# Kernel tuning notes

Measured on AMD Instinct MI355X. Metric: run time of the kernel, lower is better.

Reference implementation:

```python
import jax, jax.numpy as jnp
import numpy as np

N_NODES = 100000
N_EDGES = 1200000
N_GRAPHS = 256
IN_C, HID_C, OUT_C = 5, 64, 2


def gcn_conv(x, src, dst, W, b, n_nodes):
    """PyG GCNConv: h = x@W; add self-loops; deg from target col (edge weight 1);
    norm = deg^{-1/2}[src]*deg^{-1/2}[dst]; scatter-add messages into dst; + bias."""
    loop = jnp.arange(n_nodes, dtype=src.dtype)
    s = jnp.concatenate([src, loop])
    d = jnp.concatenate([dst, loop])
    deg = jax.ops.segment_sum(jnp.ones_like(d, dtype=x.dtype), d, num_segments=n_nodes)
    dinv = jnp.where(deg > 0, jax.lax.rsqrt(deg), 0.0)
    norm = dinv[s] * dinv[d]                     # [E+N]
    h = x @ W                                    # [N, out]
    msg = h[s] * norm[:, None]                   # gather + scale  [E+N, out]
    out = jax.ops.segment_sum(msg, d, num_segments=n_nodes)  # scatter-add
    return out + b


def setup_inputs() -> dict:
    key = jax.random.key(0)
    ks = jax.random.split(key, 10)
    x = jax.random.normal(ks[0], (N_NODES, IN_C), dtype=jnp.float32)
    edge_index = jax.random.randint(ks[1], (2, N_EDGES), 0, N_NODES, dtype=jnp.int64)
    batch = jnp.sort(jax.random.randint(ks[2], (N_NODES,), 0, N_GRAPHS, dtype=jnp.int64))
    def glorot(k, fan_in, fan_out):
        lim = np.sqrt(6.0 / (fan_in + fan_out))
        return jax.random.uniform(k, (fan_in, fan_out), jnp.float32, -lim, lim)
    W1 = glorot(ks[3], IN_C, HID_C)
    b1 = jnp.zeros((HID_C,), jnp.float32)
    W2 = glorot(ks[4], HID_C, HID_C)
    b2 = jnp.zeros((HID_C,), jnp.float32)
    Wfc = glorot(ks[5], HID_C, OUT_C)
    bfc = jnp.zeros((OUT_C,), jnp.float32)
    return {"x": x, "edge_index": edge_index, "batch": batch,
            "W1": W1, "b1": b1, "W2": W2, "b2": b2, "Wfc": Wfc, "bfc": bfc}


def reference(x, edge_index, batch, W1, b1, W2, b2, Wfc, bfc):
    src, dst = edge_index[0], edge_index[1]
    h = jax.nn.relu(gcn_conv(x, src, dst, W1, b1, N_NODES))
    h = jax.nn.relu(gcn_conv(h, src, dst, W2, b2, N_NODES))
    # global_mean_pool over graph ids in `batch`
    sums = jax.ops.segment_sum(h, batch, num_segments=N_GRAPHS)          # [G, H]
    cnts = jax.ops.segment_sum(jnp.ones((h.shape[0],), h.dtype), batch,
                               num_segments=N_GRAPHS)                    # [G]
    pooled = sums / jnp.maximum(cnts, 1.0)[:, None]
    return pooled @ Wfc + bfc                                            # [G, 2]
```

## Files before the change

### kernel.cpp

```cpp
#include <hip/hip_runtime.h>

#define N_NODES 100000
#define N_EDGES 1200000
#define N_GRAPHS 256
#define IN_C 5
#define HID_C 64
#define OUT_C 2

#define BSH 7
#define BNODES 128
#define NB ((N_NODES + BNODES - 1) / BNODES)
#define CAPB 2048
#define EPB 2048
#define NBLK_E ((N_EDGES + EPB - 1) / EPB)
#define GNPW 8
#define L1NPW 8

typedef unsigned int uint32;

__device__ __forceinline__ uint32 f2bf(float f) {
    uint32 x = __float_as_uint(f);
    return (x + 0x7FFFu + ((x >> 16) & 1u)) >> 16;
}
__device__ __forceinline__ float bflo(uint32 r) { return __uint_as_float(r << 16); }
__device__ __forceinline__ float bfhi(uint32 r) { return __uint_as_float(r & 0xFFFF0000u); }

__global__ void k_bscatter(const int* __restrict__ src, const int* __restrict__ dst,
                           int* __restrict__ bcnt, int* __restrict__ pairs,
                           float* __restrict__ pooled) {
    __shared__ int h[NB];
    if (blockIdx.x < (N_GRAPHS * HID_C) / 256)
        pooled[blockIdx.x * 256 + threadIdx.x] = 0.f;
    for (int i = threadIdx.x; i < NB; i += blockDim.x) h[i] = 0;
    __syncthreads();
    int e0 = blockIdx.x * EPB;
    int e1 = e0 + EPB; if (e1 > N_EDGES) e1 = N_EDGES;
    for (int e = e0 + threadIdx.x; e < e1; e += blockDim.x)
        atomicAdd(&h[dst[e] >> BSH], 1);
    __syncthreads();
    for (int i = threadIdx.x; i < NB; i += blockDim.x)
        if (h[i]) h[i] = (i << 11) + atomicAdd(&bcnt[i], h[i]);
    __syncthreads();
    for (int e = e0 + threadIdx.x; e < e1; e += blockDim.x) {
        int d = dst[e];
        int pos = atomicAdd(&h[d >> BSH], 1);
        pairs[pos] = ((d & (BNODES - 1)) << 17) | src[e];
    }
}

__global__ void k_bsort_xs(const int* __restrict__ pairs, const int* __restrict__ bcnt,
                           const float* __restrict__ x,
                           int* __restrict__ csr, int* __restrict__ rs,
                           int* __restrict__ cnt, float* __restrict__ dinv,
                           float* __restrict__ xs) {
    __shared__ int hist[BNODES];
    __shared__ int tmp[BNODES];
    __shared__ int cur[BNODES];
    __shared__ float sdv[BNODES];
    int b = blockIdx.x;
    int t = threadIdx.x;
    int base = b << BSH;
    if (t < BNODES) hist[t] = 0;
    __syncthreads();
    int s = b << 11;
    int n = bcnt[b];
    for (int i = t; i < n; i += 256)
        atomicAdd(&hist[pairs[s + i] >> 17], 1);
    __syncthreads();
    int v = (t < BNODES) ? hist[t] : 0;
    if (t < BNODES) tmp[t] = v;
    __syncthreads();
    for (int off = 1; off < BNODES; off <<= 1) {
        int a = (t < BNODES && t >= off) ? tmp[t - off] : 0;
        __syncthreads();
        if (t < BNODES) tmp[t] += a;
        __syncthreads();
    }
    float dv_t = rsqrtf((float)v + 1.0f);
    if (t < BNODES) {
        cur[t] = tmp[t] - v;
        sdv[t] = dv_t;
        if (base + t < N_NODES) {
            rs[base + t] = s + tmp[t] - v;
            cnt[base + t] = v;
            dinv[base + t] = dv_t;
        }
    }
    __syncthreads();
    for (int i = t; i < n; i += 256) {
        int p = pairs[s + i];
        int pos = atomicAdd(&cur[p >> 17], 1);
        csr[s + pos] = p & 0x1FFFF;
    }
    for (int i = t; i < BNODES * 8; i += 256) {
        int nl = i >> 3, k = i & 7;
        int node = base + nl;
        if (node < N_NODES && k < IN_C)
            xs[(unsigned)node * 8 + k] = x[(unsigned)node * IN_C + k] * sdv[nl];
    }
}

__global__ void __launch_bounds__(256) k_l1(
        const float* __restrict__ xs, const int* __restrict__ csr,
        const int* __restrict__ rs, const int* __restrict__ cnt,
        const float* __restrict__ dinv, const float* __restrict__ b1,
        const float* __restrict__ W1, const float* __restrict__ W2,
        uint32* __restrict__ g2t) {
    __shared__ __align__(16) float sagg[4][L1NPW][8];
    __shared__ __align__(16) float srow[4][2][HID_C];
    int tid = threadIdx.x;
    int w = tid >> 6;
    int lane = tid & 63;
    int base = (blockIdx.x * 4 + w) * L1NPW;

    int g = lane >> 3, l = lane & 7;
    int v = base + g;
    float a0 = 0.f, a1 = 0.f, a2 = 0.f, a3 = 0.f, a4 = 0.f;
    if (v < N_NODES) {
        int k0 = rs[v];
        int n = cnt[v];
        if (l == 0) {
            float4 p = *(const float4*)&xs[(unsigned)v * 8];
            a0 = p.x; a1 = p.y; a2 = p.z; a3 = p.w;
            a4 = xs[(unsigned)v * 8 + 4];
        }
        int i = l;
        int un = (i < n) ? csr[k0 + i] : -1;
        while (un >= 0) {
            int u = un;
            i += 8;
            un = (i < n) ? csr[k0 + i] : -1;
            float4 p = *(const float4*)&xs[(unsigned)u * 8];
            float p4 = xs[(unsigned)u * 8 + 4];
            a0 += p.x; a1 += p.y; a2 += p.z; a3 += p.w; a4 += p4;
        }
    }
#pragma unroll
    for (int off = 4; off; off >>= 1) {
        a0 += __shfl_xor(a0, off);
        a1 += __shfl_xor(a1, off);
        a2 += __shfl_xor(a2, off);
        a3 += __shfl_xor(a3, off);
        a4 += __shfl_xor(a4, off);
    }
    if (l == 0 && v < N_NODES) {
        *(float4*)&sagg[w][g][0] = make_float4(a0, a1, a2, a3);
        sagg[w][g][4] = a4;
    }

    int half = lane >> 5, c2 = lane & 31;
    int kb = half << 5;
    float2 w1r[IN_C];
#pragma unroll
    for (int k = 0; k < IN_C; ++k)
        w1r[k] = *(const float2*)&W1[k * HID_C + 2 * c2];
    float2 w2r[32];
#pragma unroll
    for (int j = 0; j < 32; ++j)
        w2r[j] = *(const float2*)&W2[(kb + j) * HID_C + 2 * c2];
    float2 bias = *(const float2*)&b1[2 * c2];

    for (int gg = 0; gg < L1NPW; ++gg) {
        int node = base + gg;
        if (node >= N_NODES) break;
        float dv = dinv[node];
        float4 qa = *(const float4*)&sagg[w][gg][0];
        float q4 = sagg[w][gg][4];
        float s0 = qa.x * w1r[0].x + qa.y * w1r[1].x + qa.z * w1r[2].x
                 + qa.w * w1r[3].x + q4 * w1r[4].x;
        float s1 = qa.x * w1r[0].y + qa.y * w1r[1].y + qa.z * w1r[2].y
                 + qa.w * w1r[3].y + q4 * w1r[4].y;
        float h0 = fmaxf(s0 * dv + bias.x, 0.f);
        float h1 = fmaxf(s1 * dv + bias.y, 0.f);
        int buf = gg & 1;
        if (half == 0) *(float2*)&srow[w][buf][2 * c2] = make_float2(h0, h1);
        float t0 = 0.f, t1 = 0.f;
#pragma unroll
        for (int jj = 0; jj < 8; ++jj) {
            float4 hv = *(const float4*)&srow[w][buf][kb + 4 * jj];
            t0 += hv.x * w2r[4 * jj + 0].x + hv.y * w2r[4 * jj + 1].x
                + hv.z * w2r[4 * jj + 2].x + hv.w * w2r[4 * jj + 3].x;
            t1 += hv.x * w2r[4 * jj + 0].y + hv.y * w2r[4 * jj + 1].y
                + hv.z * w2r[4 * jj + 2].y + hv.w * w2r[4 * jj + 3].y;
        }
        t0 += __shfl_xor(t0, 32);
        t1 += __shfl_xor(t1, 32);
        if (half == 0)
            g2t[(unsigned)node * 32 + c2] = (f2bf(t1 * dv) << 16) | f2bf(t0 * dv);
    }
}

#define LDU2(d, u) uint2 d = *(const uint2*)&g[(unsigned)(u) * 32 + 2 * c4]
#define ACC4(s0, s1, s2, s3, r) { s0 += bflo(r.x); s1 += bfhi(r.x); \
                                  s2 += bflo(r.y); s3 += bfhi(r.y); }
__global__ void __launch_bounds__(256, 4) k_gather2p(
        const uint32* __restrict__ g, const int* __restrict__ csr,
        const int* __restrict__ rs, const int* __restrict__ cnt,
        const float* __restrict__ dinv, const float* __restrict__ b,
        const int* __restrict__ batch, float* __restrict__ pooled) {
    int wv = __builtin_amdgcn_readfirstlane(
        blockIdx.x * (blockDim.x >> 6) + (threadIdx.x >> 6));
    int n0 = wv * GNPW;
    if (n0 >= N_NODES) return;
    int lane = threadIdx.x & 63;
    int sub = lane >> 4;
    int c4 = lane & 15;
    int va = n0 + sub, vb = n0 + 4 + sub;
    int ka = rs[va], na = cnt[va];
    int kb = rs[vb], nb = cnt[vb];
    float dva = dinv[va], dvb = dinv[vb];
    int ga = batch[va], gb = batch[vb];
    float4 bias = *(const float4*)&b[4 * c4];
    LDU2(rsa, va); LDU2(rsb, vb);
    float a0 = bflo(rsa.x), a1 = bfhi(rsa.x), a2 = bflo(rsa.y), a3 = bfhi(rsa.y);
    float y0 = bflo(rsb.x), y1 = bfhi(rsb.x), y2 = bflo(rsb.y), y3 = bfhi(rsb.y);
    int ia = 0, ib = 0;
    while (ia + 7 < na && ib + 7 < nb) {
        int u0 = csr[ka+ia+0], u1 = csr[ka+ia+1], u2 = csr[ka+ia+2], u3 = csr[ka+ia+3];
        int u4 = csr[ka+ia+4], u5 = csr[ka+ia+5], u6 = csr[ka+ia+6], u7 = csr[ka+ia+7];
        int w0 = csr[kb+ib+0], w1 = csr[kb+ib+1], w2 = csr[kb+ib+2], w3 = csr[kb+ib+3];
        int w4 = csr[kb+ib+4], w5 = csr[kb+ib+5], w6 = csr[kb+ib+6], w7 = csr[kb+ib+7];
        LDU2(p0, u0); LDU2(p1, u1); LDU2(p2, u2); LDU2(p3, u3);
        LDU2(p4, u4); LDU2(p5, u5); LDU2(p6, u6); LDU2(p7, u7);
        LDU2(q0, w0); LDU2(q1, w1); LDU2(q2, w2); LDU2(q3, w3);
        LDU2(q4, w4); LDU2(q5, w5); LDU2(q6, w6); LDU2(q7, w7);
        ACC4(a0, a1, a2, a3, p0); ACC4(a0, a1, a2, a3, p1);
        ACC4(a0, a1, a2, a3, p2); ACC4(a0, a1, a2, a3, p3);
        ACC4(a0, a1, a2, a3, p4); ACC4(a0, a1, a2, a3, p5);
        ACC4(a0, a1, a2, a3, p6); ACC4(a0, a1, a2, a3, p7);
        ACC4(y0, y1, y2, y3, q0); ACC4(y0, y1, y2, y3, q1);
        ACC4(y0, y1, y2, y3, q2); ACC4(y0, y1, y2, y3, q3);
        ACC4(y0, y1, y2, y3, q4); ACC4(y0, y1, y2, y3, q5);
        ACC4(y0, y1, y2, y3, q6); ACC4(y0, y1, y2, y3, q7);
        ia += 8; ib += 8;
    }
    while (ia + 7 < na) {
        int u0 = csr[ka+ia+0], u1 = csr[ka+ia+1], u2 = csr[ka+ia+2], u3 = csr[ka+ia+3];
        int u4 = csr[ka+ia+4], u5 = csr[ka+ia+5], u6 = csr[ka+ia+6], u7 = csr[ka+ia+7];
        LDU2(p0, u0); LDU2(p1, u1); LDU2(p2, u2); LDU2(p3, u3);
        LDU2(p4, u4); LDU2(p5, u5); LDU2(p6, u6); LDU2(p7, u7);
        ACC4(a0, a1, a2, a3, p0); ACC4(a0, a1, a2, a3, p1);
        ACC4(a0, a1, a2, a3, p2); ACC4(a0, a1, a2, a3, p3);
        ACC4(a0, a1, a2, a3, p4); ACC4(a0, a1, a2, a3, p5);
        ACC4(a0, a1, a2, a3, p6); ACC4(a0, a1, a2, a3, p7);
        ia += 8;
    }
    while (ib + 7 < nb) {
        int w0 = csr[kb+ib+0], w1 = csr[kb+ib+1], w2 = csr[kb+ib+2], w3 = csr[kb+ib+3];
        int w4 = csr[kb+ib+4], w5 = csr[kb+ib+5], w6 = csr[kb+ib+6], w7 = csr[kb+ib+7];
        LDU2(q0, w0); LDU2(q1, w1); LDU2(q2, w2); LDU2(q3, w3);
        LDU2(q4, w4); LDU2(q5, w5); LDU2(q6, w6); LDU2(q7, w7);
        ACC4(y0, y1, y2, y3, q0); ACC4(y0, y1, y2, y3, q1);
        ACC4(y0, y1, y2, y3, q2); ACC4(y0, y1, y2, y3, q3);
        ACC4(y0, y1, y2, y3, q4); ACC4(y0, y1, y2, y3, q5);
        ACC4(y0, y1, y2, y3, q6); ACC4(y0, y1, y2, y3, q7);
        ib += 8;
    }
    while (ia + 3 < na && ib + 3 < nb) {
        int u0 = csr[ka+ia+0], u1 = csr[ka+ia+1], u2 = csr[ka+ia+2], u3 = csr[ka+ia+3];
        int w0 = csr[kb+ib+0], w1 = csr[kb+ib+1], w2 = csr[kb+ib+2], w3 = csr[kb+ib+3];
        LDU2(p0, u0); LDU2(p1, u1); LDU2(p2, u2); LDU2(p3, u3);
        LDU2(q0, w0); LDU2(q1, w1); LDU2(q2, w2); LDU2(q3, w3);
        ACC4(a0, a1, a2, a3, p0); ACC4(a0, a1, a2, a3, p1);
        ACC4(a0, a1, a2, a3, p2); ACC4(a0, a1, a2, a3, p3);
        ACC4(y0, y1, y2, y3, q0); ACC4(y0, y1, y2, y3, q1);
        ACC4(y0, y1, y2, y3, q2); ACC4(y0, y1, y2, y3, q3);
        ia += 4; ib += 4;
    }
    while (ia + 3 < na) {
        int u0 = csr[ka+ia+0], u1 = csr[ka+ia+1], u2 = csr[ka+ia+2], u3 = csr[ka+ia+3];
        LDU2(p0, u0); LDU2(p1, u1); LDU2(p2, u2); LDU2(p3, u3);
        ACC4(a0, a1, a2, a3, p0); ACC4(a0, a1, a2, a3, p1);
        ACC4(a0, a1, a2, a3, p2); ACC4(a0, a1, a2, a3, p3);
        ia += 4;
    }
    while (ib + 3 < nb) {
        int w0 = csr[kb+ib+0], w1 = csr[kb+ib+1], w2 = csr[kb+ib+2], w3 = csr[kb+ib+3];
        LDU2(q0, w0); LDU2(q1, w1); LDU2(q2, w2); LDU2(q3, w3);
        ACC4(y0, y1, y2, y3, q0); ACC4(y0, y1, y2, y3, q1);
        ACC4(y0, y1, y2, y3, q2); ACC4(y0, y1, y2, y3, q3);
        ib += 4;
    }
    while (ia < na && ib < nb) {
        int u0 = csr[ka + ia], w0 = csr[kb + ib];
        LDU2(p0, u0); LDU2(q0, w0);
        ACC4(a0, a1, a2, a3, p0); ACC4(y0, y1, y2, y3, q0);
        ++ia; ++ib;
    }
    while (ia < na) {
        LDU2(p0, csr[ka + ia]);
        ACC4(a0, a1, a2, a3, p0);
        ++ia;
    }
    while (ib < nb) {
        LDU2(q0, csr[kb + ib]);
        ACC4(y0, y1, y2, y3, q0);
        ++ib;
    }
    float oa0 = fmaxf(a0 * dva + bias.x, 0.f);
    float oa1 = fmaxf(a1 * dva + bias.y, 0.f);
    float oa2 = fmaxf(a2 * dva + bias.z, 0.f);
    float oa3 = fmaxf(a3 * dva + bias.w, 0.f);
    float ob0 = fmaxf(y0 * dvb + bias.x, 0.f);
    float ob1 = fmaxf(y1 * dvb + bias.y, 0.f);
    float ob2 = fmaxf(y2 * dvb + bias.z, 0.f);
    float ob3 = fmaxf(y3 * dvb + bias.w, 0.f);
    int g0 = __builtin_amdgcn_readfirstlane(ga);
    if (__all(ga == g0) && __all(gb == g0)) {
        float f0 = oa0 + ob0, f1 = oa1 + ob1, f2 = oa2 + ob2, f3 = oa3 + ob3;
        f0 += __shfl_xor(f0, 16); f0 += __shfl_xor(f0, 32);
        f1 += __shfl_xor(f1, 16); f1 += __shfl_xor(f1, 32);
        f2 += __shfl_xor(f2, 16); f2 += __shfl_xor(f2, 32);
        f3 += __shfl_xor(f3, 16); f3 += __shfl_xor(f3, 32);
        if (sub == 0) {
            atomicAdd(&pooled[g0 * HID_C + 4 * c4 + 0], f0);
            atomicAdd(&pooled[g0 * HID_C + 4 * c4 + 1], f1);
            atomicAdd(&pooled[g0 * HID_C + 4 * c4 + 2], f2);
            atomicAdd(&pooled[g0 * HID_C + 4 * c4 + 3], f3);
        }
    } else {
        atomicAdd(&pooled[ga * HID_C + 4 * c4 + 0], oa0);
        atomicAdd(&pooled[ga * HID_C + 4 * c4 + 1], oa1);
        atomicAdd(&pooled[ga * HID_C + 4 * c4 + 2], oa2);
        atomicAdd(&pooled[ga * HID_C + 4 * c4 + 3], oa3);
        atomicAdd(&pooled[gb * HID_C + 4 * c4 + 0], ob0);
        atomicAdd(&pooled[gb * HID_C + 4 * c4 + 1], ob1);
        atomicAdd(&pooled[gb * HID_C + 4 * c4 + 2], ob2);
        atomicAdd(&pooled[gb * HID_C + 4 * c4 + 3], ob3);
    }
}

__global__ void k_fc(const float* __restrict__ pooled, const int* __restrict__ batch,
                     const float* __restrict__ Wfc, const float* __restrict__ bfc,
                     float* __restrict__ out) {
    int g = blockIdx.x;
    int c = threadIdx.x;
    int lo = 0, hi = N_NODES;
    while (lo < hi) { int mid = (lo + hi) >> 1; if (batch[mid] < g) lo = mid + 1; else hi = mid; }
    int start = lo;
    hi = N_NODES;
    while (lo < hi) { int mid = (lo + hi) >> 1; if (batch[mid] < g + 1) lo = mid + 1; else hi = mid; }
    int n = lo - start;
    float pv = pooled[g * HID_C + c] / (float)(n > 0 ? n : 1);
    float o0 = pv * Wfc[c * OUT_C + 0];
    float o1 = pv * Wfc[c * OUT_C + 1];
#pragma unroll
    for (int off = 32; off > 0; off >>= 1) {
        o0 += __shfl_down(o0, off);
        o1 += __shfl_down(o1, off);
    }
    if (c == 0) {
        out[g * OUT_C + 0] = o0 + bfc[0];
        out[g * OUT_C + 1] = o1 + bfc[1];
    }
}

extern "C" void kernel_launch(void* const* d_in, const int* in_sizes, int n_in,
                              void* d_out, int out_size, void* d_ws, size_t ws_size,
                              hipStream_t stream) {
    const float* x    = (const float*)d_in[0];
    const int*   ei   = (const int*)d_in[1];
    const int*   src  = ei;
    const int*   dst  = ei + N_EDGES;
    const int*   batch= (const int*)d_in[2];
    const float* W1   = (const float*)d_in[3];
    const float* b1   = (const float*)d_in[4];
    const float* W2   = (const float*)d_in[5];
    const float* b2   = (const float*)d_in[6];
    const float* Wfc  = (const float*)d_in[7];
    const float* bfc  = (const float*)d_in[8];
    float* out = (float*)d_out;

    float*  ws     = (float*)d_ws;
    int*    bcnt   = (int*)ws;
    float*  pooled = ws + 1024;
    float*  dinv   = pooled + 16384;
    int*    cnt    = (int*)(dinv + 100352);
    int*    rs     = cnt + 100352;
    int*    pairs  = rs + 100352;
    int*    csr    = pairs + (NB * CAPB);
    float*  xs     = (float*)(csr + (NB * CAPB));
    uint32* g2tab  = (uint32*)(xs + N_NODES * 8);

    hipMemsetAsync(bcnt, 0, 1024 * sizeof(int), stream);

    k_bscatter<<<NBLK_E, 256, 0, stream>>>(src, dst, bcnt, pairs, pooled);
    k_bsort_xs<<<NB, 256, 0, stream>>>(pairs, bcnt, x, csr, rs, cnt, dinv, xs);

    {
        int blocks = (N_NODES + 4 * L1NPW - 1) / (4 * L1NPW);
        k_l1<<<blocks, 256, 0, stream>>>(xs, csr, rs, cnt, dinv, b1, W1, W2, g2tab);
    }

    {
        int waves = (N_NODES + GNPW - 1) / GNPW;
        int blocks = (waves + 3) / 4;
        k_gather2p<<<blocks, 256, 0, stream>>>(g2tab, csr, rs, cnt, dinv, b2, batch, pooled);
    }

    k_fc<<<N_GRAPHS, 64, 0, stream>>>(pooled, batch, Wfc, bfc, out);
}
```

Measured before the change: 205.0 us.

## Split layer-2 feature table into channel slices mapped to XCD pairs

The bf16 layer-2 feature table is stored as four 16-channel slices instead of one 64-channel row per node. The gather kernel maps blocks so that each pair of XCDs handles one slice, which shrinks the working set each XCD's L2 must cache during random neighbour gathers. Each wave now processes 32 nodes with 4 lanes per node rather than 8 nodes with 16 lanes. The cost is four times as many CSR index reads and edge loops, plus extra shuffle reductions before the pooled atomics.

```diff
diff --git a/kernel.cpp b/kernel.cpp
--- a/kernel.cpp
+++ b/kernel.cpp
@@ -13,8 +13,8 @@
 #define CAPB 2048
 #define EPB 2048
 #define NBLK_E ((N_EDGES + EPB - 1) / EPB)
-#define GNPW 8
 #define L1NPW 8
+#define SLICE_W (N_NODES * 8)
 
 typedef unsigned int uint32;
 
@@ -159,6 +159,8 @@
     for (int j = 0; j < 32; ++j)
         w2r[j] = *(const float2*)&W2[(kb + j) * HID_C + 2 * c2];
     float2 bias = *(const float2*)&b1[2 * c2];
+    unsigned sbase = (unsigned)(c2 >> 3) * SLICE_W;
+    int wir = c2 & 7;
 
     for (int gg = 0; gg < L1NPW; ++gg) {
         int node = base + gg;
@@ -186,34 +188,41 @@
         t0 += __shfl_xor(t0, 32);
         t1 += __shfl_xor(t1, 32);
         if (half == 0)
-            g2t[(unsigned)node * 32 + c2] = (f2bf(t1 * dv) << 16) | f2bf(t0 * dv);
-    }
-}
-
-#define LDU2(d, u) uint2 d = *(const uint2*)&g[(unsigned)(u) * 32 + 2 * c4]
+            g2t[sbase + (unsigned)node * 8 + wir] = (f2bf(t1 * dv) << 16) | f2bf(t0 * dv);
+    }
+}
+
+#define LDU2(d, u) uint2 d = *(const uint2*)&gs[(unsigned)(u) * 8 + 2 * cq]
 #define ACC4(s0, s1, s2, s3, r) { s0 += bflo(r.x); s1 += bfhi(r.x); \
                                   s2 += bflo(r.y); s3 += bfhi(r.y); }
 __global__ void __launch_bounds__(256, 4) k_gather2p(
-        const uint32* __restrict__ g, const int* __restrict__ csr,
+        const uint32* __restrict__ g2s, const int* __restrict__ csr,
         const int* __restrict__ rs, const int* __restrict__ cnt,
         const float* __restrict__ dinv, const float* __restrict__ b,
         const int* __restrict__ batch, float* __restrict__ pooled) {
-    int wv = __builtin_amdgcn_readfirstlane(
-        blockIdx.x * (blockDim.x >> 6) + (threadIdx.x >> 6));
-    int n0 = wv * GNPW;
-    if (n0 >= N_NODES) return;
+    int blk = blockIdx.x;
+    int xcd = blk & 7;
+    int slice = xcd >> 1;
+    int sblk = ((blk >> 3) << 1) | (xcd & 1);
+    int w = threadIdx.x >> 6;
     int lane = threadIdx.x & 63;
-    int sub = lane >> 4;
-    int c4 = lane & 15;
-    int va = n0 + sub, vb = n0 + 4 + sub;
-    int ka = rs[va], na = cnt[va];
-    int kb = rs[vb], nb = cnt[vb];
-    float dva = dinv[va], dvb = dinv[vb];
-    int ga = batch[va], gb = batch[vb];
-    float4 bias = *(const float4*)&b[4 * c4];
-    LDU2(rsa, va); LDU2(rsb, vb);
-    float a0 = bflo(rsa.x), a1 = bfhi(rsa.x), a2 = bflo(rsa.y), a3 = bfhi(rsa.y);
-    float y0 = bflo(rsb.x), y1 = bfhi(rsb.x), y2 = bflo(rsb.y), y3 = bfhi(rsb.y);
+    int sub = lane >> 2;
+    int cq = lane & 3;
+    int n0 = sblk * BNODES + w * 32;
+    int va = n0 + sub, vb = n0 + 16 + sub;
+    int vva = va < N_NODES, vvb = vb < N_NODES;
+    int vca = vva ? va : N_NODES - 1;
+    int vcb = vvb ? vb : N_NODES - 1;
+    const uint32* gs = g2s + (unsigned)slice * SLICE_W;
+    int ka = rs[vca], na = vva ? cnt[vca] : 0;
+    int kb = rs[vcb], nb = vvb ? cnt[vcb] : 0;
+    float dva = dinv[vca], dvb = dinv[vcb];
+    int ga = batch[vca], gb = batch[vcb];
+    float4 bias = *(const float4*)&b[slice * 16 + 4 * cq];
+    float a0 = 0.f, a1 = 0.f, a2 = 0.f, a3 = 0.f;
+    float y0 = 0.f, y1 = 0.f, y2 = 0.f, y3 = 0.f;
+    if (vva) { LDU2(rsa, va); ACC4(a0, a1, a2, a3, rsa); }
+    if (vvb) { LDU2(rsb, vb); ACC4(y0, y1, y2, y3, rsb); }
     int ia = 0, ib = 0;
     while (ia + 7 < na && ib + 7 < nb) {
         int u0 = csr[ka+ia+0], u1 = csr[ka+ia+1], u2 = csr[ka+ia+2], u3 = csr[ka+ia+3];
@@ -297,36 +306,41 @@
         ACC4(y0, y1, y2, y3, q0);
         ++ib;
     }
-    float oa0 = fmaxf(a0 * dva + bias.x, 0.f);
-    float oa1 = fmaxf(a1 * dva + bias.y, 0.f);
-    float oa2 = fmaxf(a2 * dva + bias.z, 0.f);
-    float oa3 = fmaxf(a3 * dva + bias.w, 0.f);
-    float ob0 = fmaxf(y0 * dvb + bias.x, 0.f);
-    float ob1 = fmaxf(y1 * dvb + bias.y, 0.f);
-    float ob2 = fmaxf(y2 * dvb + bias.z, 0.f);
-    float ob3 = fmaxf(y3 * dvb + bias.w, 0.f);
+    float oa0 = vva ? fmaxf(a0 * dva + bias.x, 0.f) : 0.f;
+    float oa1 = vva ? fmaxf(a1 * dva + bias.y, 0.f) : 0.f;
+    float oa2 = vva ? fmaxf(a2 * dva + bias.z, 0.f) : 0.f;
+    float oa3 = vva ? fmaxf(a3 * dva + bias.w, 0.f) : 0.f;
+    float ob0 = vvb ? fmaxf(y0 * dvb + bias.x, 0.f) : 0.f;
+    float ob1 = vvb ? fmaxf(y1 * dvb + bias.y, 0.f) : 0.f;
+    float ob2 = vvb ? fmaxf(y2 * dvb + bias.z, 0.f) : 0.f;
+    float ob3 = vvb ? fmaxf(y3 * dvb + bias.w, 0.f) : 0.f;
     int g0 = __builtin_amdgcn_readfirstlane(ga);
+    int cb = slice * 16 + 4 * cq;
     if (__all(ga == g0) && __all(gb == g0)) {
         float f0 = oa0 + ob0, f1 = oa1 + ob1, f2 = oa2 + ob2, f3 = oa3 + ob3;
+        f0 += __shfl_xor(f0, 4); f0 += __shfl_xor(f0, 8);
         f0 += __shfl_xor(f0, 16); f0 += __shfl_xor(f0, 32);
+        f1 += __shfl_xor(f1, 4); f1 += __shfl_xor(f1, 8);
         f1 += __shfl_xor(f1, 16); f1 += __shfl_xor(f1, 32);
+        f2 += __shfl_xor(f2, 4); f2 += __shfl_xor(f2, 8);
         f2 += __shfl_xor(f2, 16); f2 += __shfl_xor(f2, 32);
+        f3 += __shfl_xor(f3, 4); f3 += __shfl_xor(f3, 8);
         f3 += __shfl_xor(f3, 16); f3 += __shfl_xor(f3, 32);
         if (sub == 0) {
-            atomicAdd(&pooled[g0 * HID_C + 4 * c4 + 0], f0);
-            atomicAdd(&pooled[g0 * HID_C + 4 * c4 + 1], f1);
-            atomicAdd(&pooled[g0 * HID_C + 4 * c4 + 2], f2);
-            atomicAdd(&pooled[g0 * HID_C + 4 * c4 + 3], f3);
+            atomicAdd(&pooled[g0 * HID_C + cb + 0], f0);
+            atomicAdd(&pooled[g0 * HID_C + cb + 1], f1);
+            atomicAdd(&pooled[g0 * HID_C + cb + 2], f2);
+            atomicAdd(&pooled[g0 * HID_C + cb + 3], f3);
         }
     } else {
-        atomicAdd(&pooled[ga * HID_C + 4 * c4 + 0], oa0);
-        atomicAdd(&pooled[ga * HID_C + 4 * c4 + 1], oa1);
-        atomicAdd(&pooled[ga * HID_C + 4 * c4 + 2], oa2);
-        atomicAdd(&pooled[ga * HID_C + 4 * c4 + 3], oa3);
-        atomicAdd(&pooled[gb * HID_C + 4 * c4 + 0], ob0);
-        atomicAdd(&pooled[gb * HID_C + 4 * c4 + 1], ob1);
-        atomicAdd(&pooled[gb * HID_C + 4 * c4 + 2], ob2);
-        atomicAdd(&pooled[gb * HID_C + 4 * c4 + 3], ob3);
+        atomicAdd(&pooled[ga * HID_C + cb + 0], oa0);
+        atomicAdd(&pooled[ga * HID_C + cb + 1], oa1);
+        atomicAdd(&pooled[ga * HID_C + cb + 2], oa2);
+        atomicAdd(&pooled[ga * HID_C + cb + 3], oa3);
+        atomicAdd(&pooled[gb * HID_C + cb + 0], ob0);
+        atomicAdd(&pooled[gb * HID_C + cb + 1], ob1);
+        atomicAdd(&pooled[gb * HID_C + cb + 2], ob2);
+        atomicAdd(&pooled[gb * HID_C + cb + 3], ob3);
     }
 }
 
@@ -392,11 +406,7 @@
         k_l1<<<blocks, 256, 0, stream>>>(xs, csr, rs, cnt, dinv, b1, W1, W2, g2tab);
     }
 
-    {
-        int waves = (N_NODES + GNPW - 1) / GNPW;
-        int blocks = (waves + 3) / 4;
-        k_gather2p<<<blocks, 256, 0, stream>>>(g2tab, csr, rs, cnt, dinv, b2, batch, pooled);
-    }
+    k_gather2p<<<NB * 4, 256, 0, stream>>>(g2tab, csr, rs, cnt, dinv, b2, batch, pooled);
 
     k_fc<<<N_GRAPHS, 64, 0, stream>>>(pooled, batch, Wfc, bfc, out);
 }
```

Result: slower. 228.0 us (+11.2%).

## Build CSR via global degree count, three-pass scan and atomic placement

Applied to the files above, without the earlier changes.

Replaces the two-level bucket sort (block histogram scatter into fixed 2048-slot buckets, then per-bucket local sort) with a classic CSR build. It counts degrees with global atomics, computes prefix sums in three kernels, and places edges with a global atomic cursor per node. This drops the intermediate pairs buffer and its fixed capacity, but adds more kernel launches and heavy global atomics on a random destination array, and edge order within each row becomes nondeterministic.

```diff
diff --git a/kernel.cpp b/kernel.cpp
--- a/kernel.cpp
+++ b/kernel.cpp
@@ -7,12 +7,9 @@
 #define HID_C 64
 #define OUT_C 2
 
-#define BSH 7
-#define BNODES 128
-#define NB ((N_NODES + BNODES - 1) / BNODES)
-#define CAPB 2048
 #define EPB 2048
 #define NBLK_E ((N_EDGES + EPB - 1) / EPB)
+#define NBP ((N_NODES + 255) / 256)
 #define GNPW 8
 #define L1NPW 8
 
@@ -25,78 +22,86 @@
 __device__ __forceinline__ float bflo(uint32 r) { return __uint_as_float(r << 16); }
 __device__ __forceinline__ float bfhi(uint32 r) { return __uint_as_float(r & 0xFFFF0000u); }
 
-__global__ void k_bscatter(const int* __restrict__ src, const int* __restrict__ dst,
-                           int* __restrict__ bcnt, int* __restrict__ pairs,
-                           float* __restrict__ pooled) {
-    __shared__ int h[NB];
+__global__ void k_deg(const int* __restrict__ dst, int* __restrict__ deg,
+                      float* __restrict__ pooled) {
     if (blockIdx.x < (N_GRAPHS * HID_C) / 256)
         pooled[blockIdx.x * 256 + threadIdx.x] = 0.f;
-    for (int i = threadIdx.x; i < NB; i += blockDim.x) h[i] = 0;
-    __syncthreads();
     int e0 = blockIdx.x * EPB;
     int e1 = e0 + EPB; if (e1 > N_EDGES) e1 = N_EDGES;
     for (int e = e0 + threadIdx.x; e < e1; e += blockDim.x)
-        atomicAdd(&h[dst[e] >> BSH], 1);
+        atomicAdd(&deg[dst[e]], 1);
+}
+
+__global__ void k_scanA(const int* __restrict__ deg, int* __restrict__ partials) {
+    __shared__ int sm[4];
+    int t = threadIdx.x;
+    int node = blockIdx.x * 256 + t;
+    int d = (node < N_NODES) ? deg[node] : 0;
+#pragma unroll
+    for (int off = 32; off > 0; off >>= 1) d += __shfl_down(d, off);
+    if ((t & 63) == 0) sm[t >> 6] = d;
     __syncthreads();
-    for (int i = threadIdx.x; i < NB; i += blockDim.x)
-        if (h[i]) h[i] = (i << 11) + atomicAdd(&bcnt[i], h[i]);
+    if (t == 0) partials[blockIdx.x] = sm[0] + sm[1] + sm[2] + sm[3];
+}
+
+__global__ void k_scanB(const int* __restrict__ partials, int* __restrict__ boff) {
+    __shared__ int sm[512];
+    int t = threadIdx.x;
+    int v = (t < NBP) ? partials[t] : 0;
+    sm[t] = v;
     __syncthreads();
+    for (int off = 1; off < 512; off <<= 1) {
+        int a = (t >= off) ? sm[t - off] : 0;
+        __syncthreads();
+        sm[t] += a;
+        __syncthreads();
+    }
+    if (t < NBP) boff[t] = sm[t] - v;
+}
+
+__global__ void k_scanC(const int* __restrict__ deg, const int* __restrict__ boff,
+                        const float* __restrict__ x, int* __restrict__ rs,
+                        int* __restrict__ cur, float* __restrict__ dinv,
+                        float* __restrict__ xs) {
+    __shared__ int sm[256];
+    __shared__ float sdv[256];
+    int b = blockIdx.x, t = threadIdx.x;
+    int node = b * 256 + t;
+    int d = (node < N_NODES) ? deg[node] : 0;
+    sm[t] = d;
+    __syncthreads();
+    for (int off = 1; off < 256; off <<= 1) {
+        int a = (t >= off) ? sm[t - off] : 0;
+        __syncthreads();
+        sm[t] += a;
+        __syncthreads();
+    }
+    int excl = sm[t] - d;
+    int base = boff[b];
+    float dv = rsqrtf((float)d + 1.0f);
+    sdv[t] = dv;
+    if (node < N_NODES) {
+        rs[node] = base + excl;
+        cur[node] = base + excl;
+        dinv[node] = dv;
+    }
+    __syncthreads();
+    for (int i = t; i < 256 * 8; i += 256) {
+        int nl = i >> 3, k = i & 7;
+        int nd = b * 256 + nl;
+        if (nd < N_NODES && k < IN_C)
+            xs[(unsigned)nd * 8 + k] = x[(unsigned)nd * IN_C + k] * sdv[nl];
+    }
+}
+
+__global__ void k_place(const int* __restrict__ src, const int* __restrict__ dst,
+                        int* __restrict__ cur, int* __restrict__ csr) {
+    int e0 = blockIdx.x * EPB;
+    int e1 = e0 + EPB; if (e1 > N_EDGES) e1 = N_EDGES;
     for (int e = e0 + threadIdx.x; e < e1; e += blockDim.x) {
         int d = dst[e];
-        int pos = atomicAdd(&h[d >> BSH], 1);
-        pairs[pos] = ((d & (BNODES - 1)) << 17) | src[e];
-    }
-}
-
-__global__ void k_bsort_xs(const int* __restrict__ pairs, const int* __restrict__ bcnt,
-                           const float* __restrict__ x,
-                           int* __restrict__ csr, int* __restrict__ rs,
-                           int* __restrict__ cnt, float* __restrict__ dinv,
-                           float* __restrict__ xs) {
-    __shared__ int hist[BNODES];
-    __shared__ int tmp[BNODES];
-    __shared__ int cur[BNODES];
-    __shared__ float sdv[BNODES];
-    int b = blockIdx.x;
-    int t = threadIdx.x;
-    int base = b << BSH;
-    if (t < BNODES) hist[t] = 0;
-    __syncthreads();
-    int s = b << 11;
-    int n = bcnt[b];
-    for (int i = t; i < n; i += 256)
-        atomicAdd(&hist[pairs[s + i] >> 17], 1);
-    __syncthreads();
-    int v = (t < BNODES) ? hist[t] : 0;
-    if (t < BNODES) tmp[t] = v;
-    __syncthreads();
-    for (int off = 1; off < BNODES; off <<= 1) {
-        int a = (t < BNODES && t >= off) ? tmp[t - off] : 0;
-        __syncthreads();
-        if (t < BNODES) tmp[t] += a;
-        __syncthreads();
-    }
-    float dv_t = rsqrtf((float)v + 1.0f);
-    if (t < BNODES) {
-        cur[t] = tmp[t] - v;
-        sdv[t] = dv_t;
-        if (base + t < N_NODES) {
-            rs[base + t] = s + tmp[t] - v;
-            cnt[base + t] = v;
-            dinv[base + t] = dv_t;
-        }
-    }
-    __syncthreads();
-    for (int i = t; i < n; i += 256) {
-        int p = pairs[s + i];
-        int pos = atomicAdd(&cur[p >> 17], 1);
-        csr[s + pos] = p & 0x1FFFF;
-    }
-    for (int i = t; i < BNODES * 8; i += 256) {
-        int nl = i >> 3, k = i & 7;
-        int node = base + nl;
-        if (node < N_NODES && k < IN_C)
-            xs[(unsigned)node * 8 + k] = x[(unsigned)node * IN_C + k] * sdv[nl];
+        int pos = atomicAdd(&cur[d], 1);
+        csr[pos] = src[e];
     }
 }
 
@@ -371,31 +376,35 @@
     const float* bfc  = (const float*)d_in[8];
     float* out = (float*)d_out;
 
-    float*  ws     = (float*)d_ws;
-    int*    bcnt   = (int*)ws;
-    float*  pooled = ws + 1024;
-    float*  dinv   = pooled + 16384;
-    int*    cnt    = (int*)(dinv + 100352);
-    int*    rs     = cnt + 100352;
-    int*    pairs  = rs + 100352;
-    int*    csr    = pairs + (NB * CAPB);
-    float*  xs     = (float*)(csr + (NB * CAPB));
-    uint32* g2tab  = (uint32*)(xs + N_NODES * 8);
-
-    hipMemsetAsync(bcnt, 0, 1024 * sizeof(int), stream);
-
-    k_bscatter<<<NBLK_E, 256, 0, stream>>>(src, dst, bcnt, pairs, pooled);
-    k_bsort_xs<<<NB, 256, 0, stream>>>(pairs, bcnt, x, csr, rs, cnt, dinv, xs);
+    float*  ws      = (float*)d_ws;
+    float*  pooled  = ws;
+    int*    deg     = (int*)(ws + 16384);
+    int*    rsx     = deg + 100352;
+    int*    curx    = rsx + 100352;
+    float*  dinv    = (float*)(curx + 100352);
+    int*    partials= (int*)(dinv + 100352);
+    int*    boff    = partials + 1024;
+    int*    csr     = boff + 1024;
+    float*  xs      = (float*)(csr + 1200128);
+    uint32* g2tab   = (uint32*)(xs + N_NODES * 8);
+
+    hipMemsetAsync(deg, 0, 100352 * sizeof(int), stream);
+
+    k_deg<<<NBLK_E, 256, 0, stream>>>(dst, deg, pooled);
+    k_scanA<<<NBP, 256, 0, stream>>>(deg, partials);
+    k_scanB<<<1, 512, 0, stream>>>(partials, boff);
+    k_scanC<<<NBP, 256, 0, stream>>>(deg, boff, x, rsx, curx, dinv, xs);
+    k_place<<<NBLK_E, 256, 0, stream>>>(src, dst, curx, csr);
 
     {
         int blocks = (N_NODES + 4 * L1NPW - 1) / (4 * L1NPW);
-        k_l1<<<blocks, 256, 0, stream>>>(xs, csr, rs, cnt, dinv, b1, W1, W2, g2tab);
+        k_l1<<<blocks, 256, 0, stream>>>(xs, csr, rsx, deg, dinv, b1, W1, W2, g2tab);
     }
 
     {
         int waves = (N_NODES + GNPW - 1) / GNPW;
         int blocks = (waves + 3) / 4;
-        k_gather2p<<<blocks, 256, 0, stream>>>(g2tab, csr, rs, cnt, dinv, b2, batch, pooled);
+        k_gather2p<<<blocks, 256, 0, stream>>>(g2tab, csr, rsx, deg, dinv, b2, batch, pooled);
     }
 
     k_fc<<<N_GRAPHS, 64, 0, stream>>>(pooled, batch, Wfc, bfc, out);
```

Result: slower. 324.4 us (+58.3%).
